# Performance work log

Hardware: AMD Instinct MI355X
Metric: run time of the kernel (lower is better)

## Reference

```python
import jax, jax.numpy as jnp
import numpy as np


def setup_inputs() -> dict:
    key = jax.random.key(0)
    ks = jax.random.split(key, 6)
    B, C, H, W = 8, 128, 48, 64
    return {
        "feature0": jax.random.normal(ks[0], (B, C, H, W), dtype=jnp.float32),
        "feature1": jax.random.normal(ks[1], (B, C, H, W), dtype=jnp.float32),
        "q_w": jax.random.normal(ks[2], (C, C), dtype=jnp.float32) * 0.05,
        "q_b": jax.random.normal(ks[3], (C,), dtype=jnp.float32) * 0.05,
        "k_w": jax.random.normal(ks[4], (C, C), dtype=jnp.float32) * 0.05,
        "k_b": jax.random.normal(ks[5], (C,), dtype=jnp.float32) * 0.05,
        "scale_idx": 0,
    }


def reference(feature0, feature1, q_w, q_b, k_w, k_b, scale_idx):
    # scale_idx=0 -> corr_radius=-1 (global correlation), prop_radius=-1 (global self-attn)
    b, c, h, w = feature0.shape
    n = h * w
    inv_sqrt_c = 1.0 / jnp.sqrt(jnp.asarray(c, feature0.dtype))

    f0 = feature0.reshape(b, c, n).transpose(0, 2, 1)  # [B, N, C]
    f1 = feature1.reshape(b, c, n)                     # [B, C, N]

    corr = jnp.einsum('bnc,bcm->bnm', f0, f1) * inv_sqrt_c  # [B, N, N]
    prob = jax.nn.softmax(corr, axis=-1)
    ys, xs = jnp.meshgrid(jnp.arange(h, dtype=feature0.dtype),
                          jnp.arange(w, dtype=feature0.dtype), indexing='ij')
    grid = jnp.stack([xs, ys], axis=-1).reshape(n, 2)        # [N, 2] (x, y)
    correspondence = jnp.einsum('bnm,md->bnd', prob, grid)   # [B, N, 2]
    flow_pred = (correspondence - grid[None]).reshape(b, h, w, 2).transpose(0, 3, 1, 2)  # [B,2,H,W]

    # ---- SelfAttnPropagation (global): q = q_proj(f0), k = k_proj(q) ----
    q = f0 @ q_w.T + q_b              # [B, N, C]
    k = q @ k_w.T + k_b               # [B, N, C]  (projected from q, per unimatch)
    scores = jnp.einsum('bnc,bmc->bnm', q, k) * inv_sqrt_c
    attn = jax.nn.softmax(scores, axis=-1)
    v = jax.lax.stop_gradient(flow_pred).reshape(b, 2, n).transpose(0, 2, 1)  # [B, N, 2]
    flow = jnp.einsum('bnm,bmd->bnd', attn, v).reshape(b, h, w, 2).transpose(0, 3, 1, 2)

    return flow, flow_pred
```

## Files before the change

kernel.cpp:

```cpp
#include <hip/hip_runtime.h>

constexpr int BATCH = 8;
constexpr int CH    = 128;
constexpr int NPix  = 3072;
constexpr int NT    = 48;
constexpr int NCHUNK = 4;
constexpr int TPC   = NT / NCHUNK;
constexpr int MPC   = TPC * 64;
constexpr int TILE_SHORTS = 64 * CH;
constexpr float INV_SQRT_C = 0.08838834764831845f;

typedef __bf16 bf16x8 __attribute__((ext_vector_type(8)));
typedef float  floatx4 __attribute__((ext_vector_type(4)));

static __device__ __forceinline__ unsigned short f2bf(float f) {
  unsigned int u = __float_as_uint(f);
  u += 0x7fff + ((u >> 16) & 1);
  return (unsigned short)(u >> 16);
}
static __device__ __forceinline__ float bf2f(unsigned short h) {
  return __uint_as_float((unsigned int)h << 16);
}

static __device__ __forceinline__ void loadT(float (*T)[65],
                                             const float* __restrict__ src, int t) {
  const int cc = 4 * (t & 15);
  const int kb = t >> 4;
#pragma unroll
  for (int p = 0; p < 8; ++p) {
    const int k = kb + 16 * p;
    const float4 v = *(const float4*)(src + (size_t)k * NPix + cc);
    T[k][cc] = v.x; T[k][cc + 1] = v.y; T[k][cc + 2] = v.z; T[k][cc + 3] = v.w;
  }
}

__global__ __launch_bounds__(256) void w2_kernel(
    const float* __restrict__ qw, const float* __restrict__ qb,
    const float* __restrict__ kw, const float* __restrict__ kb,
    float* __restrict__ W2, float* __restrict__ b2) {
  const int t = threadIdx.x;
  const int o = blockIdx.x * 2 + (t >> 7);
  const int i = t & 127;
  float acc = 0.f;
#pragma unroll 8
  for (int j = 0; j < CH; ++j)
    acc = fmaf(kw[o * CH + j], qw[j * CH + i], acc);
  W2[o * CH + i] = acc;
  if (i == 0) {
    float a2 = kb[o];
#pragma unroll 8
    for (int j = 0; j < CH; ++j) a2 = fmaf(kw[o * CH + j], qb[j], a2);
    b2[o] = a2;
  }
}

__global__ __launch_bounds__(256) void wfrag_kernel(
    const float* __restrict__ qw, const float* __restrict__ W2,
    unsigned short* __restrict__ qwb_hi, unsigned short* __restrict__ qwb_lo,
    unsigned short* __restrict__ w2b_hi, unsigned short* __restrict__ w2b_lo) {
  const int t = threadIdx.x;
  const bool second = blockIdx.x >= 8;
  const int cidx = (blockIdx.x & 7) * 256 + t;
  const int lane = cidx & 63, kc = (cidx >> 6) & 3, cb = cidx >> 8;
  const int co  = cb * 16 + (lane & 15);
  const int ci0 = kc * 32 + (lane >> 4) * 8;
  const float* src = (second ? W2 : qw) + co * CH + ci0;
  unsigned short vh[8], vl[8];
#pragma unroll
  for (int j = 0; j < 8; ++j) {
    const float v = src[j];
    const unsigned short h = f2bf(v);
    vh[j] = h;
    vl[j] = f2bf(v - bf2f(h));
  }
  *(uint4*)((second ? w2b_hi : qwb_hi) + (size_t)cidx * 8) = *(uint4*)vh;
  *(uint4*)((second ? w2b_lo : qwb_lo) + (size_t)cidx * 8) = *(uint4*)vl;
}

__global__ __launch_bounds__(256, 3) void preproc_kernel(
    const float* __restrict__ f0, const float* __restrict__ f1,
    const float* __restrict__ qb, const float* __restrict__ b2,
    const unsigned short* __restrict__ qwb_hi, const unsigned short* __restrict__ qwb_lo,
    const unsigned short* __restrict__ w2b_hi, const unsigned short* __restrict__ w2b_lo,
    unsigned short* __restrict__ f0t, unsigned short* __restrict__ f1t,
    unsigned short* __restrict__ qt, unsigned short* __restrict__ kt) {
  __shared__ float T[CH][65];
  const int t = threadIdx.x;
  const bool isF0 = blockIdx.x >= BATCH * NT;
  const int bi = blockIdx.x - (isF0 ? BATCH * NT : 0);
  const int b = bi / NT, tile = bi % NT;
  const size_t tb = (size_t)bi * TILE_SHORTS;

  loadT(T, (isF0 ? f0 : f1) + (size_t)b * CH * NPix + tile * 64, t);
  __syncthreads();

  unsigned short* gdst = (isF0 ? f0t : f1t) + tb;
#pragma unroll
  for (int i = 0; i < 4; ++i) {
    const int oi   = i * 256 + t;
    const int lane2 = oi & 63;
    const int kc   = (oi >> 6) & 3;
    const int c    = oi >> 8;
    const int r    = c * 16 + (lane2 & 15);
    const int ch0  = kc * 32 + (lane2 >> 4) * 8;
    unsigned short v[8];
#pragma unroll
    for (int j = 0; j < 8; ++j) v[j] = f2bf(T[ch0 + j][r]);
    *(uint4*)(gdst + (size_t)oi * 8) = *(uint4*)v;
  }
  if (!isF0) return;

  const int lane = t & 63, wave = t >> 6, quad = lane >> 4, lrow = lane & 15;

  bf16x8 ah[4], al[4];
#pragma unroll
  for (int kc = 0; kc < 4; ++kc) {
    unsigned short vh[8], vl[8];
#pragma unroll
    for (int j = 0; j < 8; ++j) {
      const float v = T[kc * 32 + quad * 8 + j][wave * 16 + lrow];
      const unsigned short h = f2bf(v);
      vh[j] = h;
      vl[j] = f2bf(v - bf2f(h));
    }
    ah[kc] = *(bf16x8*)vh;
    al[kc] = *(bf16x8*)vl;
  }

#pragma unroll
  for (int mat = 0; mat < 2; ++mat) {
    const unsigned short* wh = mat ? w2b_hi : qwb_hi;
    const unsigned short* wl = mat ? w2b_lo : qwb_lo;
    const float* bias = mat ? b2 : qb;
    unsigned short* dst = (mat ? kt : qt) + tb;
#pragma unroll
    for (int cb = 0; cb < 8; ++cb) {
      floatx4 acc = {0.f, 0.f, 0.f, 0.f};
#pragma unroll
      for (int kc = 0; kc < 4; ++kc) {
        const bf16x8 bh = *(const bf16x8*)(wh + ((cb * 4 + kc) * 64 + lane) * 8);
        const bf16x8 bl = *(const bf16x8*)(wl + ((cb * 4 + kc) * 64 + lane) * 8);
        acc = __builtin_amdgcn_mfma_f32_16x16x32_bf16(ah[kc], bh, acc, 0, 0, 0);
        acc = __builtin_amdgcn_mfma_f32_16x16x32_bf16(al[kc], bh, acc, 0, 0, 0);
        acc = __builtin_amdgcn_mfma_f32_16x16x32_bf16(ah[kc], bl, acc, 0, 0, 0);
      }
      const int co = cb * 16 + lrow;
      const float bv = bias[co];
      const int kcq = co >> 5, l2hi = ((co >> 3) & 3) * 16, j = co & 7;
#pragma unroll
      for (int r = 0; r < 4; ++r) {
        const int rl = quad * 4 + r;
        dst[((wave * 4 + kcq) * 64 + l2hi + rl) * 8 + j] = f2bf(acc[r] + bv);
      }
    }
  }
}

__global__ __launch_bounds__(256, 6) void corr_part_kernel(
    const unsigned short* __restrict__ f0t, const unsigned short* __restrict__ f1t,
    float* __restrict__ P) {
  __shared__ unsigned short Ks[TILE_SHORTS];
  const int t = threadIdx.x;
  const int b = blockIdx.x / (NT * NCHUNK);
  const int rem = blockIdx.x % (NT * NCHUNK);
  const int tile = rem >> 2, chunk = rem & 3;
  const int lane = t & 63, wave = t >> 6, quad = lane >> 4, lrow = lane & 15;

  const unsigned short* qp = f0t + (size_t)(b * NT + tile) * TILE_SHORTS;
  bf16x8 af[4];
#pragma unroll
  for (int kc = 0; kc < 4; ++kc)
    af[kc] = *(const bf16x8*)(qp + ((wave * 4 + kc) * 64 + lane) * 8);

  float l[4] = {0, 0, 0, 0}, sx[4] = {0, 0, 0, 0}, sy[4] = {0, 0, 0, 0};

  for (int mi = 0; mi < TPC; ++mi) {
    const int mt = chunk * TPC + mi;
    const unsigned short* src = f1t + (size_t)(b * NT + mt) * TILE_SHORTS;
    __syncthreads();
#pragma unroll
    for (int i = 0; i < 4; ++i)
      *(uint4*)&Ks[(i * 256 + t) * 8] = *(const uint4*)(src + (size_t)(i * 256 + t) * 8);
    __syncthreads();

    float ts[4] = {0, 0, 0, 0};
#pragma unroll
    for (int c = 0; c < 4; ++c) {
      floatx4 acc = {0.f, 0.f, 0.f, 0.f};
#pragma unroll
      for (int kc = 0; kc < 4; ++kc) {
        const bf16x8 bf = *(const bf16x8*)&Ks[((c * 4 + kc) * 64 + lane) * 8];
        acc = __builtin_amdgcn_mfma_f32_16x16x32_bf16(af[kc], bf, acc, 0, 0, 0);
      }
      const float x = (float)(c * 16 + lrow);
#pragma unroll
      for (int r = 0; r < 4; ++r) {
        const float e = __expf(acc[r] * INV_SQRT_C);
        ts[r] += e;
        sx[r] = fmaf(e, x, sx[r]);
      }
    }
    const float y = (float)mt;
#pragma unroll
    for (int r = 0; r < 4; ++r) {
      l[r] += ts[r];
      sy[r] = fmaf(y, ts[r], sy[r]);
    }
  }

#pragma unroll
  for (int off = 1; off < 16; off <<= 1)
#pragma unroll
    for (int r = 0; r < 4; ++r) {
      l[r] += __shfl_xor(l[r], off);
      sx[r] += __shfl_xor(sx[r], off);
      sy[r] += __shfl_xor(sy[r], off);
    }
  if (lrow == 0) {
#pragma unroll
    for (int r = 0; r < 4; ++r) {
      const int g = (b * NT + tile) * 64 + wave * 16 + quad * 4 + r;
      P[(g * 3 + 0) * 4 + chunk] = l[r];
      P[(g * 3 + 1) * 4 + chunk] = sx[r];
      P[(g * 3 + 2) * 4 + chunk] = sy[r];
    }
  }
}

__global__ __launch_bounds__(256, 6) void attn_part_kernel(
    const unsigned short* __restrict__ qt, const unsigned short* __restrict__ kt,
    const float* __restrict__ P, float* __restrict__ flow_pred,
    float* __restrict__ P2) {
  __shared__ unsigned short Ks[TILE_SHORTS];
  __shared__ float FP[MPC][2];
  const int t = threadIdx.x;
  const int b = blockIdx.x / (NT * NCHUNK);
  const int rem = blockIdx.x % (NT * NCHUNK);
  const int tile = rem >> 2, chunk = rem & 3;
  const int lane = t & 63, wave = t >> 6, quad = lane >> 4, lrow = lane & 15;

  for (int rr = t; rr < MPC; rr += 256) {
    const int n = chunk * MPC + rr;
    const int g = b * NPix + n;
    const float4 lv = *(const float4*)&P[(g * 3 + 0) * 4];
    const float4 xv = *(const float4*)&P[(g * 3 + 1) * 4];
    const float4 yv = *(const float4*)&P[(g * 3 + 2) * 4];
    const float lsum = (lv.x + lv.y) + (lv.z + lv.w);
    const float inv = 1.f / lsum;
    FP[rr][0] = ((xv.x + xv.y) + (xv.z + xv.w)) * inv - (float)(n & 63);
    FP[rr][1] = ((yv.x + yv.y) + (yv.z + yv.w)) * inv - (float)(n >> 6);
  }
  __syncthreads();

  if (tile == 0) {
    for (int rr = t; rr < MPC; rr += 256) {
      const int n = chunk * MPC + rr;
      flow_pred[(size_t)(b * 2 + 0) * NPix + n] = FP[rr][0];
      flow_pred[(size_t)(b * 2 + 1) * NPix + n] = FP[rr][1];
    }
  }

  const unsigned short* qp = qt + (size_t)(b * NT + tile) * TILE_SHORTS;
  bf16x8 af[4];
#pragma unroll
  for (int kc = 0; kc < 4; ++kc)
    af[kc] = *(const bf16x8*)(qp + ((wave * 4 + kc) * 64 + lane) * 8);

  float l[4] = {0, 0, 0, 0}, sx[4] = {0, 0, 0, 0}, sy[4] = {0, 0, 0, 0};

  for (int mi = 0; mi < TPC; ++mi) {
    const int mt = chunk * TPC + mi;
    const unsigned short* src = kt + (size_t)(b * NT + mt) * TILE_SHORTS;
    __syncthreads();
#pragma unroll
    for (int i = 0; i < 4; ++i)
      *(uint4*)&Ks[(i * 256 + t) * 8] = *(const uint4*)(src + (size_t)(i * 256 + t) * 8);
    __syncthreads();

#pragma unroll
    for (int c = 0; c < 4; ++c) {
      floatx4 acc = {0.f, 0.f, 0.f, 0.f};
#pragma unroll
      for (int kc = 0; kc < 4; ++kc) {
        const bf16x8 bf = *(const bf16x8*)&Ks[((c * 4 + kc) * 64 + lane) * 8];
        acc = __builtin_amdgcn_mfma_f32_16x16x32_bf16(af[kc], bf, acc, 0, 0, 0);
      }
      const int mloc = mi * 64 + c * 16 + lrow;
      const float vx = FP[mloc][0], vy = FP[mloc][1];
#pragma unroll
      for (int r = 0; r < 4; ++r) {
        const float e = __expf(acc[r] * INV_SQRT_C);
        l[r] += e;
        sx[r] = fmaf(e, vx, sx[r]);
        sy[r] = fmaf(e, vy, sy[r]);
      }
    }
  }

#pragma unroll
  for (int off = 1; off < 16; off <<= 1)
#pragma unroll
    for (int r = 0; r < 4; ++r) {
      l[r] += __shfl_xor(l[r], off);
      sx[r] += __shfl_xor(sx[r], off);
      sy[r] += __shfl_xor(sy[r], off);
    }
  if (lrow == 0) {
#pragma unroll
    for (int r = 0; r < 4; ++r) {
      const int g = (b * NT + tile) * 64 + wave * 16 + quad * 4 + r;
      P2[(g * 3 + 0) * 4 + chunk] = l[r];
      P2[(g * 3 + 1) * 4 + chunk] = sx[r];
      P2[(g * 3 + 2) * 4 + chunk] = sy[r];
    }
  }
}

__global__ __launch_bounds__(256) void reduce_attn_kernel(
    const float* __restrict__ P2, float* __restrict__ flow) {
  const int g = blockIdx.x * 256 + threadIdx.x;
  const float4 lv = *(const float4*)&P2[(g * 3 + 0) * 4];
  const float4 xv = *(const float4*)&P2[(g * 3 + 1) * 4];
  const float4 yv = *(const float4*)&P2[(g * 3 + 2) * 4];
  const float l = (lv.x + lv.y) + (lv.z + lv.w);
  const float inv = 1.f / l;
  const int b = g / NPix, n = g % NPix;
  flow[(size_t)(b * 2 + 0) * NPix + n] = ((xv.x + xv.y) + (xv.z + xv.w)) * inv;
  flow[(size_t)(b * 2 + 1) * NPix + n] = ((yv.x + yv.y) + (yv.z + yv.w)) * inv;
}

extern "C" void kernel_launch(void* const* d_in, const int* in_sizes, int n_in,
                              void* d_out, int out_size, void* d_ws,
                              size_t ws_size, hipStream_t stream) {
  const float* f0  = (const float*)d_in[0];
  const float* f1  = (const float*)d_in[1];
  const float* q_w = (const float*)d_in[2];
  const float* q_b = (const float*)d_in[3];
  const float* k_w = (const float*)d_in[4];
  const float* k_b = (const float*)d_in[5];

  float* out       = (float*)d_out;
  float* flow      = out;
  float* flow_pred = out + (size_t)BATCH * 2 * NPix;

  const size_t tile_elems = (size_t)BATCH * NT * TILE_SHORTS;
  unsigned short* f0t = (unsigned short*)d_ws;
  unsigned short* f1t = f0t + tile_elems;
  unsigned short* qt  = f1t + tile_elems;
  unsigned short* kt  = qt + tile_elems;
  unsigned short* qwb_hi = kt + tile_elems;
  unsigned short* qwb_lo = qwb_hi + 2048 * 8;
  unsigned short* w2b_hi = qwb_lo + 2048 * 8;
  unsigned short* w2b_lo = w2b_hi + 2048 * 8;
  float* W2 = (float*)(w2b_lo + 2048 * 8);
  float* b2 = W2 + CH * CH;
  float* P  = b2 + CH;
  float* P2 = P + (size_t)BATCH * NPix * 12;

  w2_kernel<<<64, 256, 0, stream>>>(q_w, q_b, k_w, k_b, W2, b2);
  wfrag_kernel<<<16, 256, 0, stream>>>(q_w, W2, qwb_hi, qwb_lo, w2b_hi, w2b_lo);
  preproc_kernel<<<2 * BATCH * NT, 256, 0, stream>>>(
      f0, f1, q_b, b2, qwb_hi, qwb_lo, w2b_hi, w2b_lo, f0t, f1t, qt, kt);
  corr_part_kernel<<<BATCH * NT * NCHUNK, 256, 0, stream>>>(f0t, f1t, P);
  attn_part_kernel<<<BATCH * NT * NCHUNK, 256, 0, stream>>>(qt, kt, P, flow_pred, P2);
  reduce_attn_kernel<<<96, 256, 0, stream>>>(P2, flow);
}
```

Baseline: 180.2 us.

## Process two query tiles per block with double-buffered K staging

Both the correlation and attention partial kernels now handle two 64-row query tiles per block, so every K tile staged into LDS feeds twice as many MFMA products. K tiles are double-buffered in shared memory, which drops one barrier per iteration and lets the next tile load while the current one is consumed. The grid is halved and the occupancy hint drops from 6 to 3 blocks per CU to fit the doubled LDS and register use. This may reduce latency hiding across waves.

```diff
diff --git a/kernel.cpp b/kernel.cpp
--- a/kernel.cpp
+++ b/kernel.cpp
@@ -32,6 +32,14 @@
     const float4 v = *(const float4*)(src + (size_t)k * NPix + cc);
     T[k][cc] = v.x; T[k][cc + 1] = v.y; T[k][cc + 2] = v.z; T[k][cc + 3] = v.w;
   }
+}
+
+static __device__ __forceinline__ void stageK(unsigned short* __restrict__ dst,
+                                              const unsigned short* __restrict__ src,
+                                              int t) {
+#pragma unroll
+  for (int i = 0; i < 4; ++i)
+    *(uint4*)&dst[(i * 256 + t) * 8] = *(const uint4*)(src + (size_t)(i * 256 + t) * 8);
 }
 
 __global__ __launch_bounds__(256) void w2_kernel(
@@ -156,87 +164,100 @@
   }
 }
 
-__global__ __launch_bounds__(256, 6) void corr_part_kernel(
+__global__ __launch_bounds__(256, 3) void corr_part_kernel(
     const unsigned short* __restrict__ f0t, const unsigned short* __restrict__ f1t,
     float* __restrict__ P) {
-  __shared__ unsigned short Ks[TILE_SHORTS];
+  __shared__ unsigned short Ks[2][TILE_SHORTS];
   const int t = threadIdx.x;
-  const int b = blockIdx.x / (NT * NCHUNK);
-  const int rem = blockIdx.x % (NT * NCHUNK);
-  const int tile = rem >> 2, chunk = rem & 3;
+  const int b = blockIdx.x / ((NT / 2) * NCHUNK);
+  const int rem = blockIdx.x % ((NT / 2) * NCHUNK);
+  const int tp = rem >> 2, chunk = rem & 3;
   const int lane = t & 63, wave = t >> 6, quad = lane >> 4, lrow = lane & 15;
 
-  const unsigned short* qp = f0t + (size_t)(b * NT + tile) * TILE_SHORTS;
-  bf16x8 af[4];
-#pragma unroll
-  for (int kc = 0; kc < 4; ++kc)
-    af[kc] = *(const bf16x8*)(qp + ((wave * 4 + kc) * 64 + lane) * 8);
-
-  float l[4] = {0, 0, 0, 0}, sx[4] = {0, 0, 0, 0}, sy[4] = {0, 0, 0, 0};
+  bf16x8 af[2][4];
+#pragma unroll
+  for (int s = 0; s < 2; ++s) {
+    const unsigned short* qp = f0t + (size_t)(b * NT + 2 * tp + s) * TILE_SHORTS;
+#pragma unroll
+    for (int kc = 0; kc < 4; ++kc)
+      af[s][kc] = *(const bf16x8*)(qp + ((wave * 4 + kc) * 64 + lane) * 8);
+  }
+
+  float l[2][4] = {{0}}, sx[2][4] = {{0}}, sy[2][4] = {{0}};
+
+  stageK(Ks[0], f1t + (size_t)(b * NT + chunk * TPC) * TILE_SHORTS, t);
 
   for (int mi = 0; mi < TPC; ++mi) {
     const int mt = chunk * TPC + mi;
-    const unsigned short* src = f1t + (size_t)(b * NT + mt) * TILE_SHORTS;
     __syncthreads();
-#pragma unroll
-    for (int i = 0; i < 4; ++i)
-      *(uint4*)&Ks[(i * 256 + t) * 8] = *(const uint4*)(src + (size_t)(i * 256 + t) * 8);
-    __syncthreads();
-
-    float ts[4] = {0, 0, 0, 0};
+    if (mi + 1 < TPC)
+      stageK(Ks[(mi + 1) & 1],
+             f1t + (size_t)(b * NT + mt + 1) * TILE_SHORTS, t);
+    const unsigned short* KB = Ks[mi & 1];
+
+    float ts[2][4] = {{0}};
 #pragma unroll
     for (int c = 0; c < 4; ++c) {
-      floatx4 acc = {0.f, 0.f, 0.f, 0.f};
-#pragma unroll
-      for (int kc = 0; kc < 4; ++kc) {
-        const bf16x8 bf = *(const bf16x8*)&Ks[((c * 4 + kc) * 64 + lane) * 8];
-        acc = __builtin_amdgcn_mfma_f32_16x16x32_bf16(af[kc], bf, acc, 0, 0, 0);
-      }
       const float x = (float)(c * 16 + lrow);
 #pragma unroll
-      for (int r = 0; r < 4; ++r) {
-        const float e = __expf(acc[r] * INV_SQRT_C);
-        ts[r] += e;
-        sx[r] = fmaf(e, x, sx[r]);
+      for (int s = 0; s < 2; ++s) {
+        floatx4 acc = {0.f, 0.f, 0.f, 0.f};
+#pragma unroll
+        for (int kc = 0; kc < 4; ++kc) {
+          const bf16x8 bf = *(const bf16x8*)&KB[((c * 4 + kc) * 64 + lane) * 8];
+          acc = __builtin_amdgcn_mfma_f32_16x16x32_bf16(af[s][kc], bf, acc, 0, 0, 0);
+        }
+#pragma unroll
+        for (int r = 0; r < 4; ++r) {
+          const float e = __expf(acc[r] * INV_SQRT_C);
+          ts[s][r] += e;
+          sx[s][r] = fmaf(e, x, sx[s][r]);
+        }
       }
     }
     const float y = (float)mt;
 #pragma unroll
-    for (int r = 0; r < 4; ++r) {
-      l[r] += ts[r];
-      sy[r] = fmaf(y, ts[r], sy[r]);
-    }
+    for (int s = 0; s < 2; ++s)
+#pragma unroll
+      for (int r = 0; r < 4; ++r) {
+        l[s][r] += ts[s][r];
+        sy[s][r] = fmaf(y, ts[s][r], sy[s][r]);
+      }
   }
 
 #pragma unroll
   for (int off = 1; off < 16; off <<= 1)
 #pragma unroll
-    for (int r = 0; r < 4; ++r) {
-      l[r] += __shfl_xor(l[r], off);
-      sx[r] += __shfl_xor(sx[r], off);
-      sy[r] += __shfl_xor(sy[r], off);
-    }
+    for (int s = 0; s < 2; ++s)
+#pragma unroll
+      for (int r = 0; r < 4; ++r) {
+        l[s][r] += __shfl_xor(l[s][r], off);
+        sx[s][r] += __shfl_xor(sx[s][r], off);
+        sy[s][r] += __shfl_xor(sy[s][r], off);
+      }
   if (lrow == 0) {
 #pragma unroll
-    for (int r = 0; r < 4; ++r) {
-      const int g = (b * NT + tile) * 64 + wave * 16 + quad * 4 + r;
-      P[(g * 3 + 0) * 4 + chunk] = l[r];
-      P[(g * 3 + 1) * 4 + chunk] = sx[r];
-      P[(g * 3 + 2) * 4 + chunk] = sy[r];
-    }
-  }
-}
-
-__global__ __launch_bounds__(256, 6) void attn_part_kernel(
+    for (int s = 0; s < 2; ++s)
+#pragma unroll
+      for (int r = 0; r < 4; ++r) {
+        const int g = (b * NT + 2 * tp + s) * 64 + wave * 16 + quad * 4 + r;
+        P[(g * 3 + 0) * 4 + chunk] = l[s][r];
+        P[(g * 3 + 1) * 4 + chunk] = sx[s][r];
+        P[(g * 3 + 2) * 4 + chunk] = sy[s][r];
+      }
+  }
+}
+
+__global__ __launch_bounds__(256, 3) void attn_part_kernel(
     const unsigned short* __restrict__ qt, const unsigned short* __restrict__ kt,
     const float* __restrict__ P, float* __restrict__ flow_pred,
     float* __restrict__ P2) {
-  __shared__ unsigned short Ks[TILE_SHORTS];
+  __shared__ unsigned short Ks[2][TILE_SHORTS];
   __shared__ float FP[MPC][2];
   const int t = threadIdx.x;
-  const int b = blockIdx.x / (NT * NCHUNK);
-  const int rem = blockIdx.x % (NT * NCHUNK);
-  const int tile = rem >> 2, chunk = rem & 3;
+  const int b = blockIdx.x / ((NT / 2) * NCHUNK);
+  const int rem = blockIdx.x % ((NT / 2) * NCHUNK);
+  const int tp = rem >> 2, chunk = rem & 3;
   const int lane = t & 63, wave = t >> 6, quad = lane >> 4, lrow = lane & 15;
 
   for (int rr = t; rr < MPC; rr += 256) {
@@ -250,9 +271,9 @@
     FP[rr][0] = ((xv.x + xv.y) + (xv.z + xv.w)) * inv - (float)(n & 63);
     FP[rr][1] = ((yv.x + yv.y) + (yv.z + yv.w)) * inv - (float)(n >> 6);
   }
-  __syncthreads();
-
-  if (tile == 0) {
+
+  if (tp == 0) {
+    __syncthreads();
     for (int rr = t; rr < MPC; rr += 256) {
       const int n = chunk * MPC + rr;
       flow_pred[(size_t)(b * 2 + 0) * NPix + n] = FP[rr][0];
@@ -260,39 +281,46 @@
     }
   }
 
-  const unsigned short* qp = qt + (size_t)(b * NT + tile) * TILE_SHORTS;
-  bf16x8 af[4];
-#pragma unroll
-  for (int kc = 0; kc < 4; ++kc)
-    af[kc] = *(const bf16x8*)(qp + ((wave * 4 + kc) * 64 + lane) * 8);
-
-  float l[4] = {0, 0, 0, 0}, sx[4] = {0, 0, 0, 0}, sy[4] = {0, 0, 0, 0};
+  bf16x8 af[2][4];
+#pragma unroll
+  for (int s = 0; s < 2; ++s) {
+    const unsigned short* qp = qt + (size_t)(b * NT + 2 * tp + s) * TILE_SHORTS;
+#pragma unroll
+    for (int kc = 0; kc < 4; ++kc)
+      af[s][kc] = *(const bf16x8*)(qp + ((wave * 4 + kc) * 64 + lane) * 8);
+  }
+
+  float l[2][4] = {{0}}, sx[2][4] = {{0}}, sy[2][4] = {{0}};
+
+  stageK(Ks[0], kt + (size_t)(b * NT + chunk * TPC) * TILE_SHORTS, t);
 
   for (int mi = 0; mi < TPC; ++mi) {
     const int mt = chunk * TPC + mi;
-    const unsigned short* src = kt + (size_t)(b * NT + mt) * TILE_SHORTS;
     __syncthreads();
-#pragma unroll
-    for (int i = 0; i < 4; ++i)
-      *(uint4*)&Ks[(i * 256 + t) * 8] = *(const uint4*)(src + (size_t)(i * 256 + t) * 8);
-    __syncthreads();
+    if (mi + 1 < TPC)
+      stageK(Ks[(mi + 1) & 1],
+             kt + (size_t)(b * NT + mt + 1) * TILE_SHORTS, t);
+    const unsigned short* KB = Ks[mi & 1];
 
 #pragma unroll
     for (int c = 0; c < 4; ++c) {
-      floatx4 acc = {0.f, 0.f, 0.f, 0.f};
-#pragma unroll
-      for (int kc = 0; kc < 4; ++kc) {
-        const bf16x8 bf = *(const bf16x8*)&Ks[((c * 4 + kc) * 64 + lane) * 8];
-        acc = __builtin_amdgcn_mfma_f32_16x16x32_bf16(af[kc], bf, acc, 0, 0, 0);
-      }
       const int mloc = mi * 64 + c * 16 + lrow;
       const float vx = FP[mloc][0], vy = FP[mloc][1];
 #pragma unroll
-      for (int r = 0; r < 4; ++r) {
-        const float e = __expf(acc[r] * INV_SQRT_C);
-        l[r] += e;
-        sx[r] = fmaf(e, vx, sx[r]);
-        sy[r] = fmaf(e, vy, sy[r]);
+      for (int s = 0; s < 2; ++s) {
+        floatx4 acc = {0.f, 0.f, 0.f, 0.f};
+#pragma unroll
+        for (int kc = 0; kc < 4; ++kc) {
+          const bf16x8 bf = *(const bf16x8*)&KB[((c * 4 + kc) * 64 + lane) * 8];
+          acc = __builtin_amdgcn_mfma_f32_16x16x32_bf16(af[s][kc], bf, acc, 0, 0, 0);
+        }
+#pragma unroll
+        for (int r = 0; r < 4; ++r) {
+          const float e = __expf(acc[r] * INV_SQRT_C);
+          l[s][r] += e;
+          sx[s][r] = fmaf(e, vx, sx[s][r]);
+          sy[s][r] = fmaf(e, vy, sy[s][r]);
+        }
       }
     }
   }
@@ -300,19 +328,23 @@
 #pragma unroll
   for (int off = 1; off < 16; off <<= 1)
 #pragma unroll
-    for (int r = 0; r < 4; ++r) {
-      l[r] += __shfl_xor(l[r], off);
-      sx[r] += __shfl_xor(sx[r], off);
-      sy[r] += __shfl_xor(sy[r], off);
-    }
+    for (int s = 0; s < 2; ++s)
+#pragma unroll
+      for (int r = 0; r < 4; ++r) {
+        l[s][r] += __shfl_xor(l[s][r], off);
+        sx[s][r] += __shfl_xor(sx[s][r], off);
+        sy[s][r] += __shfl_xor(sy[s][r], off);
+      }
   if (lrow == 0) {
 #pragma unroll
-    for (int r = 0; r < 4; ++r) {
-      const int g = (b * NT + tile) * 64 + wave * 16 + quad * 4 + r;
-      P2[(g * 3 + 0) * 4 + chunk] = l[r];
-      P2[(g * 3 + 1) * 4 + chunk] = sx[r];
-      P2[(g * 3 + 2) * 4 + chunk] = sy[r];
-    }
+    for (int s = 0; s < 2; ++s)
+#pragma unroll
+      for (int r = 0; r < 4; ++r) {
+        const int g = (b * NT + 2 * tp + s) * 64 + wave * 16 + quad * 4 + r;
+        P2[(g * 3 + 0) * 4 + chunk] = l[s][r];
+        P2[(g * 3 + 1) * 4 + chunk] = sx[s][r];
+        P2[(g * 3 + 2) * 4 + chunk] = sy[s][r];
+      }
   }
 }
 
@@ -361,7 +393,8 @@
   wfrag_kernel<<<16, 256, 0, stream>>>(q_w, W2, qwb_hi, qwb_lo, w2b_hi, w2b_lo);
   preproc_kernel<<<2 * BATCH * NT, 256, 0, stream>>>(
       f0, f1, q_b, b2, qwb_hi, qwb_lo, w2b_hi, w2b_lo, f0t, f1t, qt, kt);
-  corr_part_kernel<<<BATCH * NT * NCHUNK, 256, 0, stream>>>(f0t, f1t, P);
-  attn_part_kernel<<<BATCH * NT * NCHUNK, 256, 0, stream>>>(qt, kt, P, flow_pred, P2);
+  corr_part_kernel<<<BATCH * (NT / 2) * NCHUNK, 256, 0, stream>>>(f0t, f1t, P);
+  attn_part_kernel<<<BATCH * (NT / 2) * NCHUNK, 256, 0, stream>>>(qt, kt, P,
+                                                                  flow_pred, P2);
   reduce_attn_kernel<<<96, 256, 0, stream>>>(P2, flow);
 }
```

New measurement: 167.7 us. 1.07x faster.
